# Kernel optimization log

Measured on AMD Instinct MI355X. Metric: run time of the kernel, lower is better.

Reference implementation:

```python
import math
import jax, jax.numpy as jnp
import numpy as np

INV_SQRT2 = 1.0 / math.sqrt(2.0)
TOPK = 8


def _interleave(a, b):
    # a, b: [B, T2, F] -> [B, 2*T2, F] with a at even, b at odd time indices
    B, T2, F = a.shape
    return jnp.stack([a, b], axis=2).reshape(B, 2 * T2, F)


def setup_inputs() -> dict:
    key = jax.random.key(0)
    x = jax.random.normal(key, (8, 8192, 512), dtype=jnp.float32)
    return {"x": x}


def reference(x):
    B, T, F = x.shape  # T assumed even (setup guarantees it; torch pads otherwise)
    x_even = x[:, 0::2, :]
    x_odd = x[:, 1::2, :]
    x_low = (x_even + x_odd) * INV_SQRT2   # [B, T/2, F]
    x_high = (x_even - x_odd) * INV_SQRT2  # [B, T/2, F]

    T2 = T // 2
    k = min(TOPK, T2)
    # top-k by |x_high| along time axis, per (batch, feature) column
    mag = jnp.abs(x_high).transpose(0, 2, 1)          # [B, F, T2]
    _, idx = jax.lax.top_k(mag, k)                    # [B, F, k]
    mask = jnp.zeros((B, F, T2), dtype=bool)
    mask = mask.at[jnp.arange(B)[:, None, None],
                   jnp.arange(F)[None, :, None], idx].set(True)
    mask = mask.transpose(0, 2, 1)                    # [B, T2, F]
    xh_sparse = jnp.where(mask, x_high, jnp.zeros_like(x_high))

    low_half = x_low * INV_SQRT2
    high_half = xh_sparse * INV_SQRT2
    main = _interleave(low_half, low_half)            # even: +low, odd: -0 => same
    detail_sparse = _interleave(high_half, -high_half)
    return main, detail_sparse
```

## Files before the change

### kernel.cpp

```cpp
#include <hip/hip_runtime.h>
#include <math.h>

#define B_  8
#define T_  8192
#define T2_ 4096
#define F_  512
#define F2_ 256
#define K_  8

typedef unsigned long long u64;
typedef float fvec2 __attribute__((ext_vector_type(2)));

__device__ __forceinline__ void ins8(u64 (&a)[K_], u64 k) {
    if (k <= a[K_ - 1]) return;
#pragma unroll
    for (int j = 0; j < K_; ++j) {
        u64 hi = (k > a[j]) ? k : a[j];
        u64 lo = (k > a[j]) ? a[j] : k;
        a[j] = hi;
        k = lo;
    }
}

__global__ __launch_bounds__(256) void haar_phase1(
    const fvec2* __restrict__ x2, fvec2* __restrict__ mainOut,
    fvec2* __restrict__ detOut, u64* __restrict__ cand, int S, int L)
{
    const int tx   = threadIdx.x;
    const int f2   = blockIdx.x * 64 + tx;
    const int slot = blockIdx.y * 4 + threadIdx.y;
    const int b    = blockIdx.z;
    const int t2_0 = slot * L;

    u64 a0[K_], a1[K_];
#pragma unroll
    for (int j = 0; j < K_; ++j) { a0[j] = 0; a1[j] = 0; }

    const size_t rowBase = (size_t)b * T_;
    const fvec2 z = (fvec2)0.0f;

#pragma unroll 2
    for (int t = 0; t < L; ++t) {
        const int t2 = t2_0 + t;
        const size_t re = (rowBase + 2 * (size_t)t2) * F2_ + f2;
        fvec2 e = x2[re];
        fvec2 o = x2[re + F2_];
        fvec2 low = (e + o) * 0.5f;
        __builtin_nontemporal_store(low, &mainOut[re]);
        __builtin_nontemporal_store(low, &mainOut[re + F2_]);
        __builtin_nontemporal_store(z, &detOut[re]);
        __builtin_nontemporal_store(z, &detOut[re + F2_]);
        const u64 it = (u64)(unsigned)(~t2);
        ins8(a0, ((u64)__float_as_uint(fabsf(e.x - o.x)) << 32) | it);
        ins8(a1, ((u64)__float_as_uint(fabsf(e.y - o.y)) << 32) | it);
    }

    const size_t colBase = (size_t)b * F_ + 2 * (size_t)f2;
    u64* d0 = cand + ((colBase + 0) * S + slot) * K_;
    u64* d1 = cand + ((colBase + 1) * S + slot) * K_;
#pragma unroll
    for (int j = 0; j < K_; ++j) { d0[j] = a0[j]; d1[j] = a1[j]; }
}

__global__ __launch_bounds__(256) void haar_phase2(
    const float* __restrict__ x, const u64* __restrict__ cand,
    float* __restrict__ out, int S)
{
    const int lane = threadIdx.x & 63;
    const int wv   = threadIdx.x >> 6;
    const int col  = blockIdx.x * 4 + wv;
    const int b    = col >> 9;
    const int f    = col & (F_ - 1);
    const int n    = S * K_;

    const u64* c = cand + (size_t)col * n;
    u64 a[K_];
#pragma unroll
    for (int j = 0; j < K_; ++j) a[j] = 0;
    for (int e = lane; e < n; e += 64) ins8(a, c[e]);

    u64 wkey = 0;
#pragma unroll
    for (int j = 0; j < K_; ++j) {
        u64 m = a[0];
#pragma unroll
        for (int s = 32; s > 0; s >>= 1) {
            u64 t = __shfl_xor(m, s, 64);
            m = (t > m) ? t : m;
        }
        if (a[0] == m) {
#pragma unroll
            for (int q = 0; q < K_ - 1; ++q) a[q] = a[q + 1];
            a[K_ - 1] = 0;
        }
        if (lane == j) wkey = m;
    }

    float* det = out + (size_t)B_ * T_ * F_;
    if (lane < K_) {
        const int t2 = (int)(~(unsigned)wkey);
        const size_t re = ((size_t)b * T_ + 2 * (size_t)t2) * F_ + f;
        const float e = x[re];
        const float o = x[re + F_];
        const float v = (e - o) * 0.5f;
        det[re]      = v;
        det[re + F_] = -v;
    }
}

extern "C" void kernel_launch(void* const* d_in, const int* in_sizes, int n_in,
                              void* d_out, int out_size, void* d_ws, size_t ws_size,
                              hipStream_t stream) {
    const float* x = (const float*)d_in[0];
    float* out = (float*)d_out;
    float* detail = out + (size_t)B_ * T_ * F_;

    int S = 128;
    while (S > 32 && (size_t)B_ * F_ * (size_t)S * K_ * sizeof(u64) > ws_size) S >>= 1;
    const int L = T2_ / S;
    u64* cand = (u64*)d_ws;

    dim3 gA(F2_ / 64, S / 4, B_);
    dim3 bA(64, 4, 1);
    hipLaunchKernelGGL(haar_phase1, gA, bA, 0, stream,
                       (const fvec2*)x, (fvec2*)out, (fvec2*)detail, cand, S, L);

    const int nb = (B_ * F_) / 4;
    hipLaunchKernelGGL(haar_phase2, dim3(nb), dim3(256), 0, stream,
                       x, cand, out, S);
}
```

Baseline: 398.3 us.

## Zero detail via memset, encode sign in top-k key, fix slot count

```diff
diff --git a/kernel.cpp b/kernel.cpp
--- a/kernel.cpp
+++ b/kernel.cpp
@@ -7,6 +7,8 @@
 #define F_  512
 #define F2_ 256
 #define K_  8
+#define S_  64
+#define L_  (T2_ / S_)
 
 typedef unsigned long long u64;
 typedef float fvec2 __attribute__((ext_vector_type(2)));
@@ -24,60 +26,56 @@
 
 __global__ __launch_bounds__(256) void haar_phase1(
     const fvec2* __restrict__ x2, fvec2* __restrict__ mainOut,
-    fvec2* __restrict__ detOut, u64* __restrict__ cand, int S, int L)
+    u64* __restrict__ cand)
 {
     const int tx   = threadIdx.x;
-    const int f2   = blockIdx.x * 64 + tx;
-    const int slot = blockIdx.y * 4 + threadIdx.y;
-    const int b    = blockIdx.z;
-    const int t2_0 = slot * L;
+    const int slot = blockIdx.x;
+    const int b    = blockIdx.y;
+    const int t2_0 = slot * L_;
 
     u64 a0[K_], a1[K_];
 #pragma unroll
     for (int j = 0; j < K_; ++j) { a0[j] = 0; a1[j] = 0; }
 
-    const size_t rowBase = (size_t)b * T_;
-    const fvec2 z = (fvec2)0.0f;
+    size_t re = ((size_t)b * T_ + 2 * (size_t)t2_0) * F2_ + tx;
 
 #pragma unroll 2
-    for (int t = 0; t < L; ++t) {
-        const int t2 = t2_0 + t;
-        const size_t re = (rowBase + 2 * (size_t)t2) * F2_ + f2;
-        fvec2 e = x2[re];
-        fvec2 o = x2[re + F2_];
-        fvec2 low = (e + o) * 0.5f;
-        __builtin_nontemporal_store(low, &mainOut[re]);
-        __builtin_nontemporal_store(low, &mainOut[re + F2_]);
-        __builtin_nontemporal_store(z, &detOut[re]);
-        __builtin_nontemporal_store(z, &detOut[re + F2_]);
-        const u64 it = (u64)(unsigned)(~t2);
-        ins8(a0, ((u64)__float_as_uint(fabsf(e.x - o.x)) << 32) | it);
-        ins8(a1, ((u64)__float_as_uint(fabsf(e.y - o.y)) << 32) | it);
+    for (int t = 0; t < L_; ++t) {
+        const fvec2 e = x2[re];
+        const fvec2 o = x2[re + F2_];
+        const fvec2 low = (e + o) * 0.5f;
+        mainOut[re]       = low;
+        mainOut[re + F2_] = low;
+        const unsigned dx = __float_as_uint(e.x - o.x);
+        const unsigned dy = __float_as_uint(e.y - o.y);
+        const unsigned loBase = (unsigned)(T2_ - 1 - (t2_0 + t)) << 1;
+        ins8(a0, ((u64)(dx & 0x7fffffffu) << 32) | (loBase | (dx >> 31)));
+        ins8(a1, ((u64)(dy & 0x7fffffffu) << 32) | (loBase | (dy >> 31)));
+        re += 2 * F2_;
     }
 
-    const size_t colBase = (size_t)b * F_ + 2 * (size_t)f2;
-    u64* d0 = cand + ((colBase + 0) * S + slot) * K_;
-    u64* d1 = cand + ((colBase + 1) * S + slot) * K_;
+    const size_t colBase = (size_t)b * F_ + 2 * (size_t)tx;
+    u64* d0 = cand + ((colBase + 0) * S_ + slot) * K_;
+    u64* d1 = cand + ((colBase + 1) * S_ + slot) * K_;
 #pragma unroll
     for (int j = 0; j < K_; ++j) { d0[j] = a0[j]; d1[j] = a1[j]; }
 }
 
 __global__ __launch_bounds__(256) void haar_phase2(
-    const float* __restrict__ x, const u64* __restrict__ cand,
-    float* __restrict__ out, int S)
+    const u64* __restrict__ cand, float* __restrict__ det)
 {
     const int lane = threadIdx.x & 63;
     const int wv   = threadIdx.x >> 6;
     const int col  = blockIdx.x * 4 + wv;
     const int b    = col >> 9;
     const int f    = col & (F_ - 1);
-    const int n    = S * K_;
 
-    const u64* c = cand + (size_t)col * n;
+    const u64* c = cand + (size_t)col * (S_ * K_);
     u64 a[K_];
 #pragma unroll
     for (int j = 0; j < K_; ++j) a[j] = 0;
-    for (int e = lane; e < n; e += 64) ins8(a, c[e]);
+#pragma unroll
+    for (int e = 0; e < K_; ++e) ins8(a, c[lane + 64 * e]);
 
     u64 wkey = 0;
 #pragma unroll
@@ -96,13 +94,12 @@
         if (lane == j) wkey = m;
     }
 
-    float* det = out + (size_t)B_ * T_ * F_;
     if (lane < K_) {
-        const int t2 = (int)(~(unsigned)wkey);
+        const unsigned lo = (unsigned)wkey;
+        const int t2 = T2_ - 1 - (int)(lo >> 1);
+        float v = __uint_as_float((unsigned)(wkey >> 32)) * 0.5f;
+        if (lo & 1u) v = -v;
         const size_t re = ((size_t)b * T_ + 2 * (size_t)t2) * F_ + f;
-        const float e = x[re];
-        const float o = x[re + F_];
-        const float v = (e - o) * 0.5f;
         det[re]      = v;
         det[re + F_] = -v;
     }
@@ -115,17 +112,14 @@
     float* out = (float*)d_out;
     float* detail = out + (size_t)B_ * T_ * F_;
 
-    int S = 128;
-    while (S > 32 && (size_t)B_ * F_ * (size_t)S * K_ * sizeof(u64) > ws_size) S >>= 1;
-    const int L = T2_ / S;
+    hipMemsetAsync(detail, 0, (size_t)B_ * T_ * F_ * sizeof(float), stream);
+
     u64* cand = (u64*)d_ws;
 
-    dim3 gA(F2_ / 64, S / 4, B_);
-    dim3 bA(64, 4, 1);
-    hipLaunchKernelGGL(haar_phase1, gA, bA, 0, stream,
-                       (const fvec2*)x, (fvec2*)out, (fvec2*)detail, cand, S, L);
+    hipLaunchKernelGGL(haar_phase1, dim3(S_, B_), dim3(256), 0, stream,
+                       (const fvec2*)x, (fvec2*)out, cand);
 
     const int nb = (B_ * F_) / 4;
     hipLaunchKernelGGL(haar_phase2, dim3(nb), dim3(256), 0, stream,
-                       x, cand, out, S);
+                       cand, detail);
 }
```

Result: no change. 403.9 us (+1.4%).
